# Optimization experiments

Hardware: AMD Instinct MI355X
Metric: run time of the kernel (lower is better)

Reference implementation:

```python
import jax, jax.numpy as jnp
import numpy as np
from jax import lax

B = 2
K = 3          # class_num (out_channels)
EPS = 1e-5


def group_norm(x, gamma, beta, groups):
    # x: [B, C, D, W, H]
    b, c, d, w, h = x.shape
    xg = x.reshape(b, groups, c // groups, d, w, h)
    mu = xg.mean(axis=(2, 3, 4, 5), keepdims=True)
    var = xg.var(axis=(2, 3, 4, 5), keepdims=True)
    xg = (xg - mu) * lax.rsqrt(var + EPS)
    x = xg.reshape(b, c, d, w, h)
    return x * gamma[None, :, None, None, None] + beta[None, :, None, None, None]


def setup_inputs() -> dict:
    key = jax.random.key(0)
    ks = jax.random.split(key, 16)
    s = 0.02
    inp = {
        "x_e": jax.random.normal(ks[0], (B, 128, 24, 24, 24), jnp.float32),
        "pred": jax.random.normal(ks[1], (B, 32, 96, 96, 96), jnp.float32),
        # GAP head params
        "gn_g": jnp.ones((128,), jnp.float32),
        "gn_b": jnp.zeros((128,), jnp.float32),
        "gap_w": jax.random.normal(ks[2], (256, 128, 3, 3, 3), jnp.float32) * s,
        "gap_b": jnp.zeros((256,), jnp.float32),
        # controller_first: Conv3d(512,512,1) == Linear
        "w_cf": jax.random.normal(ks[3], (512, 512), jnp.float32) * s,
        "b_cf": jnp.zeros((512,), jnp.float32),
        # controller: Conv3d(512,256,1)
        "w_c": jax.random.normal(ks[4], (256, 512), jnp.float32) * s,
        "b_c": jnp.zeros((256,), jnp.float32),
        # ProAttention(256, reduction=16): Linear(256,16) -> ReLU -> Linear(16,32)
        "w_a1": jax.random.normal(ks[5], (16, 256), jnp.float32) * s,
        "b_a1": jnp.zeros((16,), jnp.float32),
        "w_a2": jax.random.normal(ks[6], (32, 16), jnp.float32) * s,
        "b_a2": jnp.zeros((32,), jnp.float32),
        # organ embedding [K, 256]
        "emb": jax.random.normal(ks[7], (K, 256), jnp.float32),
        # three seg heads Conv3d(32,1,1): stacked [K, 32] weight, [K] bias
        "w_seg": jax.random.normal(ks[8], (K, 32), jnp.float32) * s,
        "b_seg": jnp.zeros((K,), jnp.float32),
    }
    return inp


def reference(x_e, pred, gn_g, gn_b, gap_w, gap_b, w_cf, b_cf, w_c, b_c,
              w_a1, b_a1, w_a2, b_a2, emb, w_seg, b_seg):
    # GAP(x_e.detach()): GroupNorm -> ReLU -> Conv3d(128->256, k3, s2, VALID) -> global avg pool
    xe = lax.stop_gradient(x_e)
    g = jax.nn.relu(group_norm(xe, gn_g, gn_b, groups=16))
    g = lax.conv_general_dilated(g, gap_w, window_strides=(2, 2, 2), padding="VALID",
                                 dimension_numbers=("NCDHW", "OIDHW", "NCDHW"))
    g = g + gap_b[None, :, None, None, None]
    x_feat = g.mean(axis=(2, 3, 4))                       # [B, 256]

    # per-sample: cat(repeat(x_feat), task_encoding) -> 1x1 conv heads, vectorized over B and K
    x_cond = jnp.concatenate(
        [jnp.broadcast_to(x_feat[:, None, :], (B, K, 256)),
         jnp.broadcast_to(emb[None, :, :], (B, K, 256))], axis=-1)          # [B, K, 512]
    p = jax.nn.relu(jnp.einsum("bkc,oc->bko", x_cond, w_cf) + b_cf)          # [B, K, 512]
    p_out = p                                                                 # returned as p_out in original
    c = jnp.einsum("bkc,oc->bko", p, w_c) + b_c                              # [B, K, 256]
    hid = jax.nn.relu(jnp.einsum("bkc,oc->bko", c, w_a1) + b_a1)             # [B, K, 16]
    gate = jax.nn.sigmoid(jnp.einsum("bkc,oc->bko", hid, w_a2) + b_a2)       # [B, K, 32]

    # out_k = Conv1x1_k(gate_k * pred) = sum_c gate[b,k,c]*w_seg[k,c]*pred[b,c] + b_seg[k]
    eff_w = gate * w_seg[None, :, :]                                          # [B, K, 32]
    logits = jnp.einsum("bkc,bcdwh->bkdwh", eff_w, pred) + b_seg[None, :, None, None, None]
    return logits  # [B, 3, 96, 96, 96]  (p_out available as intermediate `p`)
```

## Files before the change

### kernel.cpp

```cpp
#include <hip/hip_runtime.h>
#include <hip/hip_bf16.h>


#define NSPAT 13824
#define P4    221184

#define WS_STATSPART 0
#define WS_WINS      1024
#define WS_XF        14848
#define WS_P         15360
#define WS_C         18432
#define WS_EFFW      19968
#define WS_SINK      20160

__global__ __launch_bounds__(256) void gn_stats_part_kernel(
    const float* __restrict__ x, const float* __restrict__ gap_w,
    const float* __restrict__ w_cf, const float* __restrict__ w_c,
    float* __restrict__ ws) {
  if (blockIdx.x >= 512) {
    float s = 0.f;
    int tid = (blockIdx.x - 512) * 256 + threadIdx.x;
    const float4* g4 = (const float4*)gap_w;
    const float4* a4 = (const float4*)w_cf;
    const float4* c4 = (const float4*)w_c;
    for (int i = tid; i < 221184; i += 16384) { float4 v = g4[i]; s += v.x + v.w; }
    for (int i = tid; i < 65536;  i += 16384) { float4 v = a4[i]; s += v.x + v.w; }
    for (int i = tid; i < 32768;  i += 16384) { float4 v = c4[i]; s += v.x + v.w; }
    if (s == 1.2345e30f) ws[WS_SINK] = s;
    return;
  }
  int blk = blockIdx.x;
  const float4* p = (const float4*)(x + (size_t)blk * 6912);
  float s = 0.f, ss = 0.f;
  for (int i = threadIdx.x; i < 1728; i += 256) {
    float4 v = p[i];
    s  += v.x + v.y + v.z + v.w;
    ss += v.x*v.x + v.y*v.y + v.z*v.z + v.w*v.w;
  }
  #pragma unroll
  for (int off = 32; off; off >>= 1) {
    s  += __shfl_down(s, off);
    ss += __shfl_down(ss, off);
  }
  __shared__ float a[4], b2[4];
  int wid = threadIdx.x >> 6, lane = threadIdx.x & 63;
  if (lane == 0) { a[wid] = s; b2[wid] = ss; }
  __syncthreads();
  if (threadIdx.x == 0) {
    float2 r;
    r.x = a[0] + a[1] + a[2] + a[3];
    r.y = b2[0] + b2[1] + b2[2] + b2[3];
    ((float2*)(ws + WS_STATSPART))[blk] = r;
  }
}

__global__ __launch_bounds__(256) void gn_relu_winsum_kernel(
    const float* __restrict__ x, const float* __restrict__ gn_g,
    const float* __restrict__ gn_b, float* __restrict__ ws) {
  int blk = blockIdx.x;
  int zh = blk & 1;
  int bc = blk >> 1;
  int b = bc >> 7, c = bc & 127;
  int bg = b * 16 + (c >> 3);

  const float2* sp = (const float2*)(ws + WS_STATSPART) + bg * 16;
  float S = 0.f, SS = 0.f;
  #pragma unroll
  for (int j = 0; j < 16; j++) { float2 r = sp[j]; S += r.x; SS += r.y; }
  float mu = S * (1.f / 110592.f);
  float var = SS * (1.f / 110592.f) - mu * mu;
  float rstd = rsqrtf(var + 1e-5f);
  float ga = gn_g[c] * rstd;
  float be = gn_b[c] - mu * ga;

  __shared__ float lds[7488];
  __shared__ float part[4][27];
  int planes = zh ? 11 : 13;
  int startf = zh ? 6912 : 0;
  int nf4 = planes * 144;
  const float4* p = (const float4*)(x + (size_t)bc * NSPAT + startf);
  float4* l4 = (float4*)lds;
  for (int i = threadIdx.x; i < nf4; i += 256) {
    float4 v = p[i];
    float4 r;
    r.x = fmaxf(v.x * ga + be, 0.f);
    r.y = fmaxf(v.y * ga + be, 0.f);
    r.z = fmaxf(v.z * ga + be, 0.f);
    r.w = fmaxf(v.w * ga + be, 0.f);
    l4[i] = r;
  }
  __syncthreads();

  float acc[27];
  #pragma unroll
  for (int k = 0; k < 27; k++) acc[k] = 0.f;
  int npos = zh ? 605 : 726;
  for (int pidx = threadIdx.x; pidx < npos; pidx += 256) {
    int zl = pidx / 121, rem = pidx % 121;
    int y = rem / 11, xx = rem % 11;
    int base = zl * 1152 + y * 48 + xx * 2;
    #pragma unroll
    for (int kz = 0; kz < 3; kz++)
      #pragma unroll
      for (int ky = 0; ky < 3; ky++)
        #pragma unroll
        for (int kx = 0; kx < 3; kx++)
          acc[kz * 9 + ky * 3 + kx] += lds[base + kz * 576 + ky * 24 + kx];
  }
  #pragma unroll
  for (int k = 0; k < 27; k++)
    for (int off = 32; off; off >>= 1)
      acc[k] += __shfl_down(acc[k], off);
  int wid = threadIdx.x >> 6, lane = threadIdx.x & 63;
  if (lane == 0)
    #pragma unroll
    for (int k = 0; k < 27; k++) part[wid][k] = acc[k];
  __syncthreads();
  if (threadIdx.x < 27) {
    float v = part[0][threadIdx.x] + part[1][threadIdx.x] +
              part[2][threadIdx.x] + part[3][threadIdx.x];
    ws[WS_WINS + blk * 27 + threadIdx.x] = v;
  }
}

__global__ __launch_bounds__(256) void xfeat_kernel(
    const float* __restrict__ ws_in, const float* __restrict__ gap_w,
    const float* __restrict__ gap_b, float* __restrict__ ws_out) {
  int b = blockIdx.x >> 5;
  int oc = blockIdx.x & 31;
  __shared__ float sl[3456];
  const float* wp = ws_in + WS_WINS + b * 6912;
  for (int i = threadIdx.x; i < 3456; i += 256) {
    int c = i / 27, k = i - c * 27;
    sl[i] = wp[c * 54 + k] + wp[c * 54 + 27 + k];
  }
  __syncthreads();
  int olocal = threadIdx.x >> 5;
  int lane32 = threadIdx.x & 31;
  int o = oc * 8 + olocal;
  const float4* w4 = (const float4*)(gap_w + (size_t)o * 3456);
  const float4* s4 = (const float4*)sl;
  float acc = 0.f;
  for (int i = lane32; i < 864; i += 32) {
    float4 wv = w4[i], sv = s4[i];
    acc += wv.x * sv.x + wv.y * sv.y + wv.z * sv.z + wv.w * sv.w;
  }
  #pragma unroll
  for (int off = 16; off; off >>= 1) acc += __shfl_down(acc, off, 32);
  if (lane32 == 0) ws_out[WS_XF + b * 256 + o] = acc * (1.f / 1331.f) + gap_b[o];
}

__global__ __launch_bounds__(256) void ctrl1_kernel(
    const float* __restrict__ ws_in, const float* __restrict__ emb,
    const float* __restrict__ w_cf, const float* __restrict__ b_cf,
    float* __restrict__ ws_out) {
  int bk = blockIdx.x >> 2;
  int q = blockIdx.x & 3;
  int b = bk / 3, k = bk % 3;
  __shared__ float cond[512];
  __shared__ float ph[2][128];
  int t = threadIdx.x;
  for (int i = t; i < 512; i += 256)
    cond[i] = (i < 256) ? ws_in[WS_XF + b * 256 + i] : emb[k * 256 + (i - 256)];
  __syncthreads();
  int ol = t & 127, half = t >> 7;
  int o = q * 128 + ol;
  const float4* w4 = (const float4*)(w_cf + (size_t)o * 512) + half * 64;
  const float4* c4 = (const float4*)cond + half * 64;
  float acc = 0.f;
  #pragma unroll 8
  for (int j = 0; j < 64; j++) {
    float4 wv = w4[j], cv = c4[j];
    acc += wv.x * cv.x + wv.y * cv.y + wv.z * cv.z + wv.w * cv.w;
  }
  ph[half][ol] = acc;
  __syncthreads();
  if (t < 128)
    ws_out[WS_P + bk * 512 + o] = fmaxf(ph[0][t] + ph[1][t] + b_cf[o], 0.f);
}

__global__ __launch_bounds__(256) void ctrl2_kernel(
    const float* __restrict__ ws_in, const float* __restrict__ w_c,
    const float* __restrict__ b_c, float* __restrict__ ws_out) {
  int bk = blockIdx.x >> 1;
  int h = blockIdx.x & 1;
  __shared__ float pbuf[512];
  __shared__ float ph[2][128];
  int t = threadIdx.x;
  for (int i = t; i < 512; i += 256) pbuf[i] = ws_in[WS_P + bk * 512 + i];
  __syncthreads();
  int ol = t & 127, half = t >> 7;
  int o = h * 128 + ol;
  const float4* w4 = (const float4*)(w_c + (size_t)o * 512) + half * 64;
  const float4* p4 = (const float4*)pbuf + half * 64;
  float acc = 0.f;
  #pragma unroll 8
  for (int j = 0; j < 64; j++) {
    float4 wv = w4[j], pv = p4[j];
    acc += wv.x * pv.x + wv.y * pv.y + wv.z * pv.z + wv.w * pv.w;
  }
  ph[half][ol] = acc;
  __syncthreads();
  if (t < 128)
    ws_out[WS_C + bk * 256 + o] = ph[0][t] + ph[1][t] + b_c[o];
}

__global__ __launch_bounds__(64) void ctrl3_kernel(
    const float* __restrict__ ws_in,
    const float* __restrict__ w_a1, const float* __restrict__ b_a1,
    const float* __restrict__ w_a2, const float* __restrict__ b_a2,
    const float* __restrict__ w_seg, float* __restrict__ ws_out) {
  int bk = blockIdx.x;
  int k = bk % 3;
  __shared__ float cbuf[256], hid[16];
  int t = threadIdx.x;
  for (int i = t; i < 256; i += 64) cbuf[i] = ws_in[WS_C + bk * 256 + i];
  __syncthreads();
  if (t < 16) {
    float acc = b_a1[t];
    const float4* w4 = (const float4*)(w_a1 + t * 256);
    const float4* c4 = (const float4*)cbuf;
    for (int j = 0; j < 64; j++) {
      float4 wv = w4[j], cv = c4[j];
      acc += wv.x * cv.x + wv.y * cv.y + wv.z * cv.z + wv.w * cv.w;
    }
    hid[t] = fmaxf(acc, 0.f);
  }
  __syncthreads();
  if (t < 32) {
    float acc = b_a2[t];
    #pragma unroll
    for (int j = 0; j < 16; j++) acc += w_a2[t * 16 + j] * hid[j];
    float gate = 1.f / (1.f + expf(-acc));
    ws_out[WS_EFFW + bk * 32 + t] = gate * w_seg[k * 32 + t];
  }
}

__global__ __launch_bounds__(256) void seg_kernel(
    const float* __restrict__ pred, const float* __restrict__ ws_in,
    const float* __restrict__ b_seg, float* __restrict__ out) {
  __shared__ float ew[192];
  if (threadIdx.x < 192) ew[threadIdx.x] = ws_in[WS_EFFW + threadIdx.x];
  __syncthreads();
  int gid = blockIdx.x * 256 + threadIdx.x;
  int b = gid / P4;
  int p = gid - b * P4;
  const float4* pr = (const float4*)pred + (size_t)b * 32 * P4 + p;
  const float* e = ew + b * 96;
  float4 a0 = {0, 0, 0, 0}, a1 = a0, a2 = a0;
  #pragma unroll 8
  for (int c = 0; c < 32; c++) {
    float4 v = pr[(size_t)c * P4];
    float w0 = e[c], w1 = e[32 + c], w2 = e[64 + c];
    a0.x += w0 * v.x; a0.y += w0 * v.y; a0.z += w0 * v.z; a0.w += w0 * v.w;
    a1.x += w1 * v.x; a1.y += w1 * v.y; a1.z += w1 * v.z; a1.w += w1 * v.w;
    a2.x += w2 * v.x; a2.y += w2 * v.y; a2.z += w2 * v.z; a2.w += w2 * v.w;
  }
  float s0 = b_seg[0], s1 = b_seg[1], s2 = b_seg[2];
  a0.x += s0; a0.y += s0; a0.z += s0; a0.w += s0;
  a1.x += s1; a1.y += s1; a1.z += s1; a1.w += s1;
  a2.x += s2; a2.y += s2; a2.z += s2; a2.w += s2;
  float4* o4 = (float4*)out + (size_t)b * 3 * P4 + p;
  o4[0]      = a0;
  o4[P4]     = a1;
  o4[2 * P4] = a2;
}

extern "C" void kernel_launch(void* const* d_in, const int* in_sizes, int n_in,
                              void* d_out, int out_size, void* d_ws, size_t ws_size,
                              hipStream_t stream) {
  const float* x_e   = (const float*)d_in[0];
  const float* pred  = (const float*)d_in[1];
  const float* gn_g  = (const float*)d_in[2];
  const float* gn_b  = (const float*)d_in[3];
  const float* gap_w = (const float*)d_in[4];
  const float* gap_b = (const float*)d_in[5];
  const float* w_cf  = (const float*)d_in[6];
  const float* b_cf  = (const float*)d_in[7];
  const float* w_c   = (const float*)d_in[8];
  const float* b_c   = (const float*)d_in[9];
  const float* w_a1  = (const float*)d_in[10];
  const float* b_a1  = (const float*)d_in[11];
  const float* w_a2  = (const float*)d_in[12];
  const float* b_a2  = (const float*)d_in[13];
  const float* emb   = (const float*)d_in[14];
  const float* w_seg = (const float*)d_in[15];
  const float* b_seg = (const float*)d_in[16];

  float* ws  = (float*)d_ws;
  float* out = (float*)d_out;

  gn_stats_part_kernel<<<576, 256, 0, stream>>>(x_e, gap_w, w_cf, w_c, ws);
  gn_relu_winsum_kernel<<<512, 256, 0, stream>>>(x_e, gn_g, gn_b, ws);
  xfeat_kernel<<<64, 256, 0, stream>>>(ws, gap_w, gap_b, ws);
  ctrl1_kernel<<<24, 256, 0, stream>>>(ws, emb, w_cf, b_cf, ws);
  ctrl2_kernel<<<12, 256, 0, stream>>>(ws, w_c, b_c, ws);
  ctrl3_kernel<<<6, 64, 0, stream>>>(ws, w_a1, b_a1, w_a2, b_a2, w_seg, ws);
  seg_kernel<<<1728, 256, 0, stream>>>(pred, ws, b_seg, out);
}
```

Baseline: 100.1 us.

## Fuse attention gate into seg kernel and make window sums separable

The ctrl3 gate MLP is folded into the segmentation kernel, with every block recomputing the six effective weight vectors from the controller output, which removes one launch. The GroupNorm window-sum kernel now processes a whole channel per block and computes the strided conv window sums separably along x, y and z instead of accumulating 27 sums per output position. The output stores become nontemporal, and the prefetch blocks also touch w_a1 and emb. The trade-off is redundant gate computation in every seg block and a larger LDS footprint in the winsum kernel.

```diff
diff --git a/kernel.cpp b/kernel.cpp
--- a/kernel.cpp
+++ b/kernel.cpp
@@ -2,30 +2,33 @@
 #include <hip/hip_bf16.h>
 
 
-#define NSPAT 13824
-#define P4    221184
+#define P4 221184
+
+typedef float v4f __attribute__((ext_vector_type(4)));
 
 #define WS_STATSPART 0
 #define WS_WINS      1024
-#define WS_XF        14848
-#define WS_P         15360
-#define WS_C         18432
-#define WS_EFFW      19968
-#define WS_SINK      20160
-
-__global__ __launch_bounds__(256) void gn_stats_part_kernel(
+#define WS_XF        7936
+#define WS_P         8448
+#define WS_C         11520
+#define WS_SINK      13056
+
+__global__ __launch_bounds__(256) void k1_stats(
     const float* __restrict__ x, const float* __restrict__ gap_w,
     const float* __restrict__ w_cf, const float* __restrict__ w_c,
+    const float* __restrict__ w_a1, const float* __restrict__ emb,
     float* __restrict__ ws) {
   if (blockIdx.x >= 512) {
     float s = 0.f;
     int tid = (blockIdx.x - 512) * 256 + threadIdx.x;
     const float4* g4 = (const float4*)gap_w;
+    for (int i = tid; i < 221184; i += 16384) { float4 v = g4[i]; s += v.x + v.w; }
     const float4* a4 = (const float4*)w_cf;
+    for (int i = tid; i < 65536;  i += 16384) { float4 v = a4[i]; s += v.x + v.w; }
     const float4* c4 = (const float4*)w_c;
-    for (int i = tid; i < 221184; i += 16384) { float4 v = g4[i]; s += v.x + v.w; }
-    for (int i = tid; i < 65536;  i += 16384) { float4 v = a4[i]; s += v.x + v.w; }
     for (int i = tid; i < 32768;  i += 16384) { float4 v = c4[i]; s += v.x + v.w; }
+    if (tid < 1024) { float4 v = ((const float4*)w_a1)[tid]; s += v.x; }
+    if (tid < 192)  { float4 v = ((const float4*)emb)[tid];  s += v.x; }
     if (s == 1.2345e30f) ws[WS_SINK] = s;
     return;
   }
@@ -54,33 +57,29 @@
   }
 }
 
-__global__ __launch_bounds__(256) void gn_relu_winsum_kernel(
+__global__ __launch_bounds__(256) void k2_winsum(
     const float* __restrict__ x, const float* __restrict__ gn_g,
     const float* __restrict__ gn_b, float* __restrict__ ws) {
+  __shared__ float stage[13824];
+  __shared__ float sx[1728];
+  __shared__ float sxy[216];
   int blk = blockIdx.x;
-  int zh = blk & 1;
-  int bc = blk >> 1;
-  int b = bc >> 7, c = bc & 127;
-  int bg = b * 16 + (c >> 3);
-
+  int c = blk & 127;
+  int bg = (blk >> 7) * 16 + (c >> 3);
   const float2* sp = (const float2*)(ws + WS_STATSPART) + bg * 16;
   float S = 0.f, SS = 0.f;
   #pragma unroll
   for (int j = 0; j < 16; j++) { float2 r = sp[j]; S += r.x; SS += r.y; }
-  float mu = S * (1.f / 110592.f);
-  float var = SS * (1.f / 110592.f) - mu * mu;
+  float mu   = S * (1.f / 110592.f);
+  float var  = SS * (1.f / 110592.f) - mu * mu;
   float rstd = rsqrtf(var + 1e-5f);
   float ga = gn_g[c] * rstd;
   float be = gn_b[c] - mu * ga;
 
-  __shared__ float lds[7488];
-  __shared__ float part[4][27];
-  int planes = zh ? 11 : 13;
-  int startf = zh ? 6912 : 0;
-  int nf4 = planes * 144;
-  const float4* p = (const float4*)(x + (size_t)bc * NSPAT + startf);
-  float4* l4 = (float4*)lds;
-  for (int i = threadIdx.x; i < nf4; i += 256) {
+  int t = threadIdx.x;
+  const float4* p = (const float4*)(x + (size_t)blk * 13824);
+  float4* l4 = (float4*)stage;
+  for (int i = t; i < 3456; i += 256) {
     float4 v = p[i];
     float4 r;
     r.x = fmaxf(v.x * ga + be, 0.f);
@@ -91,66 +90,75 @@
   }
   __syncthreads();
 
-  float acc[27];
-  #pragma unroll
-  for (int k = 0; k < 27; k++) acc[k] = 0.f;
-  int npos = zh ? 605 : 726;
-  for (int pidx = threadIdx.x; pidx < npos; pidx += 256) {
-    int zl = pidx / 121, rem = pidx % 121;
-    int y = rem / 11, xx = rem % 11;
-    int base = zl * 1152 + y * 48 + xx * 2;
+  for (int r = t; r < 576; r += 256) {
+    const float* v = stage + r * 24;
+    float e1 = 0.f, o = 0.f, e2 = 0.f;
     #pragma unroll
-    for (int kz = 0; kz < 3; kz++)
-      #pragma unroll
-      for (int ky = 0; ky < 3; ky++)
-        #pragma unroll
-        for (int kx = 0; kx < 3; kx++)
-          acc[kz * 9 + ky * 3 + kx] += lds[base + kz * 576 + ky * 24 + kx];
-  }
-  #pragma unroll
-  for (int k = 0; k < 27; k++)
-    for (int off = 32; off; off >>= 1)
-      acc[k] += __shfl_down(acc[k], off);
-  int wid = threadIdx.x >> 6, lane = threadIdx.x & 63;
-  if (lane == 0)
+    for (int xx = 0; xx < 11; xx++) {
+      e1 += v[2 * xx];
+      o  += v[2 * xx + 1];
+      e2 += v[2 * xx + 2];
+    }
+    sx[r * 3 + 0] = e1;
+    sx[r * 3 + 1] = o;
+    sx[r * 3 + 2] = e2;
+  }
+  __syncthreads();
+
+  if (t < 72) {
+    int zz = t / 3, kx = t % 3;
+    const float* v = sx + zz * 72 + kx;
+    float e1 = 0.f, o = 0.f, e2 = 0.f;
     #pragma unroll
-    for (int k = 0; k < 27; k++) part[wid][k] = acc[k];
-  __syncthreads();
-  if (threadIdx.x < 27) {
-    float v = part[0][threadIdx.x] + part[1][threadIdx.x] +
-              part[2][threadIdx.x] + part[3][threadIdx.x];
-    ws[WS_WINS + blk * 27 + threadIdx.x] = v;
-  }
-}
-
-__global__ __launch_bounds__(256) void xfeat_kernel(
+    for (int yy = 0; yy < 11; yy++) {
+      e1 += v[3 * (2 * yy)];
+      o  += v[3 * (2 * yy + 1)];
+      e2 += v[3 * (2 * yy + 2)];
+    }
+    sxy[zz * 9 + 0 + kx] = e1;
+    sxy[zz * 9 + 3 + kx] = o;
+    sxy[zz * 9 + 6 + kx] = e2;
+  }
+  __syncthreads();
+
+  if (t < 9) {
+    const float* v = sxy + t;
+    float e1 = 0.f, o = 0.f, e2 = 0.f;
+    #pragma unroll
+    for (int zz = 0; zz < 11; zz++) {
+      e1 += v[9 * (2 * zz)];
+      o  += v[9 * (2 * zz + 1)];
+      e2 += v[9 * (2 * zz + 2)];
+    }
+    ws[WS_WINS + blk * 27 + 0  + t] = e1;
+    ws[WS_WINS + blk * 27 + 9  + t] = o;
+    ws[WS_WINS + blk * 27 + 18 + t] = e2;
+  }
+}
+
+__global__ __launch_bounds__(256) void k3_xfeat(
     const float* __restrict__ ws_in, const float* __restrict__ gap_w,
     const float* __restrict__ gap_b, float* __restrict__ ws_out) {
-  int b = blockIdx.x >> 5;
-  int oc = blockIdx.x & 31;
   __shared__ float sl[3456];
-  const float* wp = ws_in + WS_WINS + b * 6912;
-  for (int i = threadIdx.x; i < 3456; i += 256) {
-    int c = i / 27, k = i - c * 27;
-    sl[i] = wp[c * 54 + k] + wp[c * 54 + 27 + k];
-  }
-  __syncthreads();
-  int olocal = threadIdx.x >> 5;
-  int lane32 = threadIdx.x & 31;
-  int o = oc * 8 + olocal;
+  int b = blockIdx.x >> 6, oc = blockIdx.x & 63;
+  int t = threadIdx.x;
+  const float* wp = ws_in + WS_WINS + b * 3456;
+  for (int i = t; i < 3456; i += 256) sl[i] = wp[i];
+  __syncthreads();
+  int o = oc * 4 + (t >> 6), lane = t & 63;
   const float4* w4 = (const float4*)(gap_w + (size_t)o * 3456);
   const float4* s4 = (const float4*)sl;
   float acc = 0.f;
-  for (int i = lane32; i < 864; i += 32) {
+  for (int i = lane; i < 864; i += 64) {
     float4 wv = w4[i], sv = s4[i];
     acc += wv.x * sv.x + wv.y * sv.y + wv.z * sv.z + wv.w * sv.w;
   }
   #pragma unroll
-  for (int off = 16; off; off >>= 1) acc += __shfl_down(acc, off, 32);
-  if (lane32 == 0) ws_out[WS_XF + b * 256 + o] = acc * (1.f / 1331.f) + gap_b[o];
-}
-
-__global__ __launch_bounds__(256) void ctrl1_kernel(
+  for (int off = 32; off; off >>= 1) acc += __shfl_down(acc, off);
+  if (lane == 0) ws_out[WS_XF + b * 256 + o] = acc * (1.f / 1331.f) + gap_b[o];
+}
+
+__global__ __launch_bounds__(256) void k4_ctrl1(
     const float* __restrict__ ws_in, const float* __restrict__ emb,
     const float* __restrict__ w_cf, const float* __restrict__ b_cf,
     float* __restrict__ ws_out) {
@@ -158,7 +166,7 @@
   int q = blockIdx.x & 3;
   int b = bk / 3, k = bk % 3;
   __shared__ float cond[512];
-  __shared__ float ph[2][128];
+  __shared__ float ph[256];
   int t = threadIdx.x;
   for (int i = t; i < 512; i += 256)
     cond[i] = (i < 256) ? ws_in[WS_XF + b * 256 + i] : emb[k * 256 + (i - 256)];
@@ -173,19 +181,19 @@
     float4 wv = w4[j], cv = c4[j];
     acc += wv.x * cv.x + wv.y * cv.y + wv.z * cv.z + wv.w * cv.w;
   }
-  ph[half][ol] = acc;
+  ph[half * 128 + ol] = acc;
   __syncthreads();
   if (t < 128)
-    ws_out[WS_P + bk * 512 + o] = fmaxf(ph[0][t] + ph[1][t] + b_cf[o], 0.f);
-}
-
-__global__ __launch_bounds__(256) void ctrl2_kernel(
+    ws_out[WS_P + bk * 512 + o] = fmaxf(ph[t] + ph[128 + t] + b_cf[o], 0.f);
+}
+
+__global__ __launch_bounds__(256) void k5_ctrl2(
     const float* __restrict__ ws_in, const float* __restrict__ w_c,
     const float* __restrict__ b_c, float* __restrict__ ws_out) {
   int bk = blockIdx.x >> 1;
   int h = blockIdx.x & 1;
   __shared__ float pbuf[512];
-  __shared__ float ph[2][128];
+  __shared__ float ph[256];
   int t = threadIdx.x;
   for (int i = t; i < 512; i += 256) pbuf[i] = ws_in[WS_P + bk * 512 + i];
   __syncthreads();
@@ -199,55 +207,54 @@
     float4 wv = w4[j], pv = p4[j];
     acc += wv.x * pv.x + wv.y * pv.y + wv.z * pv.z + wv.w * pv.w;
   }
-  ph[half][ol] = acc;
+  ph[half * 128 + ol] = acc;
   __syncthreads();
   if (t < 128)
-    ws_out[WS_C + bk * 256 + o] = ph[0][t] + ph[1][t] + b_c[o];
-}
-
-__global__ __launch_bounds__(64) void ctrl3_kernel(
-    const float* __restrict__ ws_in,
+    ws_out[WS_C + bk * 256 + o] = ph[t] + ph[128 + t] + b_c[o];
+}
+
+__global__ __launch_bounds__(256) void k6_seg(
+    const float* __restrict__ pred, const float* __restrict__ ws_in,
     const float* __restrict__ w_a1, const float* __restrict__ b_a1,
     const float* __restrict__ w_a2, const float* __restrict__ b_a2,
-    const float* __restrict__ w_seg, float* __restrict__ ws_out) {
-  int bk = blockIdx.x;
-  int k = bk % 3;
-  __shared__ float cbuf[256], hid[16];
-  int t = threadIdx.x;
-  for (int i = t; i < 256; i += 64) cbuf[i] = ws_in[WS_C + bk * 256 + i];
-  __syncthreads();
-  if (t < 16) {
-    float acc = b_a1[t];
-    const float4* w4 = (const float4*)(w_a1 + t * 256);
-    const float4* c4 = (const float4*)cbuf;
+    const float* __restrict__ w_seg, const float* __restrict__ b_seg,
+    float* __restrict__ out) {
+  __shared__ float cl[1536];
+  __shared__ float hid[96];
+  __shared__ float ew[192];
+  int t = threadIdx.x;
+  for (int i = t; i < 1536; i += 256) cl[i] = ws_in[WS_C + i];
+  __syncthreads();
+  if (t < 96) {
+    int bk = t >> 4, h = t & 15;
+    const float4* w4 = (const float4*)(w_a1 + h * 256);
+    const float4* c4 = (const float4*)(cl + bk * 256);
+    float acc = b_a1[h];
+    #pragma unroll 8
     for (int j = 0; j < 64; j++) {
       float4 wv = w4[j], cv = c4[j];
-      acc += wv.x * cv.x + wv.y * cv.y + wv.z * cv.z + wv.w * cv.w;
+      acc += wv.x*cv.x + wv.y*cv.y + wv.z*cv.z + wv.w*cv.w;
     }
-    hid[t] = fmaxf(acc, 0.f);
-  }
-  __syncthreads();
-  if (t < 32) {
-    float acc = b_a2[t];
+    hid[bk * 16 + h] = fmaxf(acc, 0.f);
+  }
+  __syncthreads();
+  if (t < 192) {
+    int bk = t >> 5, o = t & 31;
+    int k = bk - (bk >= 3) * 3;
+    float acc = b_a2[o];
     #pragma unroll
-    for (int j = 0; j < 16; j++) acc += w_a2[t * 16 + j] * hid[j];
-    float gate = 1.f / (1.f + expf(-acc));
-    ws_out[WS_EFFW + bk * 32 + t] = gate * w_seg[k * 32 + t];
-  }
-}
-
-__global__ __launch_bounds__(256) void seg_kernel(
-    const float* __restrict__ pred, const float* __restrict__ ws_in,
-    const float* __restrict__ b_seg, float* __restrict__ out) {
-  __shared__ float ew[192];
-  if (threadIdx.x < 192) ew[threadIdx.x] = ws_in[WS_EFFW + threadIdx.x];
-  __syncthreads();
-  int gid = blockIdx.x * 256 + threadIdx.x;
+    for (int j = 0; j < 16; j++) acc += w_a2[o * 16 + j] * hid[bk * 16 + j];
+    float gate = 1.f / (1.f + __expf(-acc));
+    ew[bk * 32 + o] = gate * w_seg[k * 32 + o];
+  }
+  __syncthreads();
+
+  int gid = blockIdx.x * 256 + t;
   int b = gid / P4;
   int p = gid - b * P4;
   const float4* pr = (const float4*)pred + (size_t)b * 32 * P4 + p;
   const float* e = ew + b * 96;
-  float4 a0 = {0, 0, 0, 0}, a1 = a0, a2 = a0;
+  v4f a0 = {0, 0, 0, 0}, a1 = a0, a2 = a0;
   #pragma unroll 8
   for (int c = 0; c < 32; c++) {
     float4 v = pr[(size_t)c * P4];
@@ -256,14 +263,13 @@
     a1.x += w1 * v.x; a1.y += w1 * v.y; a1.z += w1 * v.z; a1.w += w1 * v.w;
     a2.x += w2 * v.x; a2.y += w2 * v.y; a2.z += w2 * v.z; a2.w += w2 * v.w;
   }
-  float s0 = b_seg[0], s1 = b_seg[1], s2 = b_seg[2];
-  a0.x += s0; a0.y += s0; a0.z += s0; a0.w += s0;
-  a1.x += s1; a1.y += s1; a1.z += s1; a1.w += s1;
-  a2.x += s2; a2.y += s2; a2.z += s2; a2.w += s2;
-  float4* o4 = (float4*)out + (size_t)b * 3 * P4 + p;
-  o4[0]      = a0;
-  o4[P4]     = a1;
-  o4[2 * P4] = a2;
+  a0 += b_seg[0];
+  a1 += b_seg[1];
+  a2 += b_seg[2];
+  v4f* o4 = (v4f*)out + (size_t)b * 3 * P4 + p;
+  __builtin_nontemporal_store(a0, o4);
+  __builtin_nontemporal_store(a1, o4 + P4);
+  __builtin_nontemporal_store(a2, o4 + 2 * P4);
 }
 
 extern "C" void kernel_launch(void* const* d_in, const int* in_sizes, int n_in,
@@ -286,15 +292,14 @@
   const float* emb   = (const float*)d_in[14];
   const float* w_seg = (const float*)d_in[15];
   const float* b_seg = (const float*)d_in[16];
-
   float* ws  = (float*)d_ws;
   float* out = (float*)d_out;
 
-  gn_stats_part_kernel<<<576, 256, 0, stream>>>(x_e, gap_w, w_cf, w_c, ws);
-  gn_relu_winsum_kernel<<<512, 256, 0, stream>>>(x_e, gn_g, gn_b, ws);
-  xfeat_kernel<<<64, 256, 0, stream>>>(ws, gap_w, gap_b, ws);
-  ctrl1_kernel<<<24, 256, 0, stream>>>(ws, emb, w_cf, b_cf, ws);
-  ctrl2_kernel<<<12, 256, 0, stream>>>(ws, w_c, b_c, ws);
-  ctrl3_kernel<<<6, 64, 0, stream>>>(ws, w_a1, b_a1, w_a2, b_a2, w_seg, ws);
-  seg_kernel<<<1728, 256, 0, stream>>>(pred, ws, b_seg, out);
-}
+  k1_stats<<<576, 256, 0, stream>>>(x_e, gap_w, w_cf, w_c, w_a1, emb, ws);
+  k2_winsum<<<256, 256, 0, stream>>>(x_e, gn_g, gn_b, ws);
+  k3_xfeat<<<128, 256, 0, stream>>>(ws, gap_w, gap_b, ws);
+  k4_ctrl1<<<24, 256, 0, stream>>>(ws, emb, w_cf, b_cf, ws);
+  k5_ctrl2<<<12, 256, 0, stream>>>(ws, w_c, b_c, ws);
+  k6_seg<<<1728, 256, 0, stream>>>(pred, ws, w_a1, b_a1, w_a2, b_a2,
+                                   w_seg, b_seg, out);
+}
```

After: 100.9 us. Within noise of the previous version (+0.8%).
